# Kernel tuning notes

Measured on AMD Instinct MI355X. Metric: run time of the kernel, lower is better.

## Reference

```python
import jax, jax.numpy as jnp
import numpy as np

EMBED = 512
EXPAND = 1024


def setup_inputs() -> dict:
    key = jax.random.key(0)
    k1, k2, k3, k4, k5 = jax.random.split(key, 5)
    B, C, P, N = 4, EMBED, 16, 1024
    x = jax.random.normal(k1, (B, C, P, N), dtype=jnp.float32)
    # 1x1 conv weights == per-pixel linear maps over the channel dim
    Wqkv = jax.random.normal(k2, (1 + 2 * EXPAND, C), dtype=jnp.float32) * (1.0 / np.sqrt(C))
    bqkv = jax.random.normal(k3, (1 + 2 * EXPAND,), dtype=jnp.float32) * 0.01
    Wout = jax.random.normal(k4, (C, EXPAND), dtype=jnp.float32) * (1.0 / np.sqrt(EXPAND))
    bout = jax.random.normal(k5, (C,), dtype=jnp.float32) * 0.01
    return {"x": x, "Wqkv": Wqkv, "bqkv": bqkv, "Wout": Wout, "bout": bout}


def reference(x, Wqkv, bqkv, Wout, bout):
    # qkv 1x1 conv: (B,C,P,N) -> (B, 1+2E, P, N)
    qkv = jnp.einsum('oc,bcpn->bopn', Wqkv, x) + bqkv[None, :, None, None]
    E = EXPAND
    query = qkv[:, :1]            # (B,1,P,N)
    key_t = qkv[:, 1:1 + E]       # (B,E,P,N)
    value = qkv[:, 1 + E:]        # (B,E,P,N)
    # softmax over patches dim (last axis); attn_dropout p=0.0 -> identity
    context_scores = jax.nn.softmax(query, axis=-1)
    # weighted sum over N, keepdim -> (B,E,P,1)
    context_vector = jnp.sum(key_t * context_scores, axis=-1, keepdims=True)
    # broadcast gate
    out = jax.nn.relu(value) * context_vector  # (B,E,P,N)
    # out 1x1 conv back to embed channels
    out = jnp.einsum('oe,bepn->bopn', Wout, out) + bout[None, :, None, None]
    return out
```

## Files before the change

kernel.cpp:

```cpp
#include <hip/hip_runtime.h>

#define EMBED 512
#define EXPAND 1024
#define PNUM 16
#define NLEN 1024
#define CHW (PNUM * NLEN)
#define SLABS 64

typedef unsigned short u16;
typedef unsigned int u32;
typedef __bf16 bf16x8 __attribute__((ext_vector_type(8)));
typedef u16 u16x8 __attribute__((ext_vector_type(8)));
typedef float f32x4 __attribute__((ext_vector_type(4)));

__device__ __forceinline__ u16 f2bf(float f) {
  u32 u = __builtin_bit_cast(u32, f);
  return (u16)((u + 0x7FFFu + ((u >> 16) & 1u)) >> 16);
}
__device__ __forceinline__ float bf2f(u16 h) {
  return __builtin_bit_cast(float, (u32)h << 16);
}
__device__ __forceinline__ void gld16(const u16* g, u16* l) {
  __builtin_amdgcn_global_load_lds((__attribute__((address_space(1))) void*)g,
                                   (__attribute__((address_space(3))) void*)l,
                                   16, 0, 0);
}
__device__ __forceinline__ f32x4 MFMA(bf16x8 a, bf16x8 b, f32x4 c) {
  return __builtin_amdgcn_mfma_f32_16x16x32_bf16(a, b, c, 0, 0, 0);
}

__global__ __launch_bounds__(256) void k_convert_w(
    const float* __restrict__ Wqkv, const float* __restrict__ Wout,
    u16* __restrict__ WvB, u16* __restrict__ WoutB) {
  const int NV = EXPAND * EMBED;
  int idx = (blockIdx.x * 256 + threadIdx.x) * 4;
  if (idx < NV) {
    float4 v = *(const float4*)(Wqkv + (size_t)(1 + EXPAND) * EMBED + idx);
    uint2 u = make_uint2((u32)f2bf(v.x) | ((u32)f2bf(v.y) << 16),
                         (u32)f2bf(v.z) | ((u32)f2bf(v.w) << 16));
    *(uint2*)(WvB + idx) = u;
  } else {
    int j = idx - NV;
    float4 v = *(const float4*)(Wout + j);
    uint2 u = make_uint2((u32)f2bf(v.x) | ((u32)f2bf(v.y) << 16),
                         (u32)f2bf(v.z) | ((u32)f2bf(v.w) << 16));
    *(uint2*)(WoutB + j) = u;
  }
}

__global__ __launch_bounds__(256) void k_convert_x(
    const float* __restrict__ x, const float* __restrict__ Wqkv,
    float* __restrict__ q, u16* __restrict__ xbT) {
  __shared__ float qp[256];
  const int slab = blockIdx.x >> 4, ng = blockIdx.x & 15;
  const int b = slab >> 4, p = slab & 15;
  const int t = threadIdx.x, w = t >> 6, l = t & 63;
  const int n = ng * 64 + l;
  const float* xs = x + (size_t)b * (EMBED * CHW) + (size_t)p * NLEN + n;
  u16* dst = xbT + (size_t)slab * (NLEN * EMBED) + (size_t)n * EMBED;
  float qacc = 0.f;
  for (int c0 = w * 128; c0 < w * 128 + 128; c0 += 16) {
    u32 pk[8];
#pragma unroll
    for (int j = 0; j < 16; ++j) {
      float v = xs[(size_t)(c0 + j) * CHW];
      qacc += Wqkv[c0 + j] * v;
      u16 h = f2bf(v);
      pk[j >> 1] = (j & 1) ? (pk[j >> 1] | ((u32)h << 16)) : (u32)h;
    }
    uint4* d4 = (uint4*)(dst + c0);
    d4[0] = make_uint4(pk[0], pk[1], pk[2], pk[3]);
    d4[1] = make_uint4(pk[4], pk[5], pk[6], pk[7]);
  }
  qp[t] = qacc;
  __syncthreads();
  if (w == 0) q[(size_t)slab * NLEN + n] = qp[l] + qp[64 + l] + qp[128 + l] + qp[192 + l];
}

__global__ __launch_bounds__(256) void k_attn1(
    const float* __restrict__ q, const u16* __restrict__ xbT,
    float* __restrict__ ypart) {
  __shared__ float red[4];
  __shared__ float sm[256];
  __shared__ float yp[4][512];
  const int slab = blockIdx.x >> 2, qr = blockIdx.x & 3;
  const int t = threadIdx.x, w = t >> 6, l = t & 63;
  const float* qrow = q + (size_t)slab * NLEN;

  float4 q4 = ((const float4*)qrow)[t];
  float m = fmaxf(fmaxf(q4.x, q4.y), fmaxf(q4.z, q4.w));
#pragma unroll
  for (int sh = 32; sh; sh >>= 1) m = fmaxf(m, __shfl_xor(m, sh, 64));
  if (l == 0) red[w] = m;
  __syncthreads();
  float gm = fmaxf(fmaxf(red[0], red[1]), fmaxf(red[2], red[3]));
  float s = __expf(q4.x - gm) + __expf(q4.y - gm) + __expf(q4.z - gm) + __expf(q4.w - gm);
#pragma unroll
  for (int sh = 32; sh; sh >>= 1) s += __shfl_xor(s, sh, 64);
  __syncthreads();
  if (l == 0) red[w] = s;
  __syncthreads();
  float gs = red[0] + red[1] + red[2] + red[3];
  sm[t] = __expf(qrow[qr * 256 + t] - gm) / gs;
  __syncthreads();

  float ya[8] = {0.f, 0.f, 0.f, 0.f, 0.f, 0.f, 0.f, 0.f};
  const u16* xs = xbT + (size_t)slab * (NLEN * EMBED) + (size_t)qr * 256 * EMBED;
  for (int ni = 0; ni < 64; ++ni) {
    const int nloc = ni * 4 + w;
    const float sc = sm[nloc];
    u16x8 v = *(const u16x8*)(xs + (size_t)nloc * EMBED + l * 8);
#pragma unroll
    for (int j = 0; j < 8; ++j) ya[j] += sc * bf2f(v[j]);
  }
#pragma unroll
  for (int j = 0; j < 8; ++j) yp[w][l * 8 + j] = ya[j];
  __syncthreads();
  for (int c = t; c < 512; c += 256)
    ypart[((size_t)slab * 4 + qr) * 512 + c] = yp[0][c] + yp[1][c] + yp[2][c] + yp[3][c];
}

__global__ __launch_bounds__(256) void k_attn2(
    const float* __restrict__ ypart, const float* __restrict__ Wqkv,
    const float* __restrict__ bqkv, float* __restrict__ cv) {
  __shared__ float yl[512];
  const int slab = blockIdx.x >> 2, ec = blockIdx.x & 3;
  const int t = threadIdx.x;
  const int e = ec * 256 + t;
  const float* yb = ypart + (size_t)slab * 4 * 512;
  for (int c = t; c < 512; c += 256)
    yl[c] = yb[c] + yb[512 + c] + yb[1024 + c] + yb[1536 + c];
  __syncthreads();
  const float* wk = Wqkv + (size_t)(1 + e) * EMBED;
  float a = 0.f;
#pragma unroll 4
  for (int c0 = 0; c0 < EMBED; c0 += 4) {
    float4 wv = *(const float4*)(wk + c0);
    a += wv.x * yl[c0] + wv.y * yl[c0 + 1] + wv.z * yl[c0 + 2] + wv.w * yl[c0 + 3];
  }
  cv[(size_t)slab * EXPAND + e] = a + bqkv[1 + e];
}

template <int K, int NT>
__device__ __forceinline__ void gemm256(const u16* __restrict__ Abase,
                                        const u16* __restrict__ Bbase,
                                        u16* lds, f32x4 (&acc)[8][4]) {
  const int t = threadIdx.x;
  const int w = t >> 6, l = t & 63;
  const int wr = w >> 2, wc = w & 3;
  const int lr = l & 15, lj = l >> 4;
  const int rowA0 = wr * 128 + lr;
  const int rowB0 = wc * 64 + lr;

  auto stage = [&](u16* dstBase, const u16* gBase, int kt) {
#pragma unroll
    for (int i = 0; i < 4; ++i) {
      const int s = i * 512 + t;
      const int row = s >> 3;
      const int pch = s & 7;
      gld16(gBase + (size_t)row * K + kt + ((pch ^ (row & 7)) << 3),
            dstBase + s * 8);
    }
  };
  auto rdA = [&](const u16* bufA, int mi, int kc) -> bf16x8 {
    const int row = rowA0 + mi * 16;
    const int ch = kc * 4 + lj;
    return *(const bf16x8*)(bufA + row * 64 + ((ch ^ (row & 7)) << 3));
  };
  auto rdB = [&](const u16* bufB, int ni, int kc) -> bf16x8 {
    const int row = rowB0 + ni * 16;
    const int ch = kc * 4 + lj;
    return *(const bf16x8*)(bufB + row * 64 + ((ch ^ (row & 7)) << 3));
  };

  stage(lds, Abase, 0);
  stage(lds + 16384, Bbase, 0);
  stage(lds + 32768, Abase, 64);
  stage(lds + 49152, Bbase, 64);
  asm volatile("s_waitcnt vmcnt(8)" ::: "memory");
  __builtin_amdgcn_s_barrier();
  __builtin_amdgcn_sched_barrier(0);

#pragma unroll 1
  for (int kt = 0; kt < NT; ++kt) {
    u16* bufA = lds + (kt & 1) * 32768;
    u16* bufB = bufA + 16384;
    const bool st = (kt + 2) < NT;
    const int kt2 = (kt + 2) * 64;
    bf16x8 a0[4][2], a1[4][2], b0[2][2], b1[2][2];

#pragma unroll
    for (int mi = 0; mi < 4; ++mi)
#pragma unroll
      for (int kc = 0; kc < 2; ++kc) a0[mi][kc] = rdA(bufA, mi, kc);
#pragma unroll
    for (int ni = 0; ni < 2; ++ni)
#pragma unroll
      for (int kc = 0; kc < 2; ++kc) b0[ni][kc] = rdB(bufB, ni, kc);
    __builtin_amdgcn_s_barrier();
    __builtin_amdgcn_sched_barrier(0);
    __builtin_amdgcn_s_setprio(1);
#pragma unroll
    for (int mi = 0; mi < 4; ++mi)
#pragma unroll
      for (int ni = 0; ni < 2; ++ni)
#pragma unroll
        for (int kc = 0; kc < 2; ++kc)
          acc[mi][ni] = MFMA(a0[mi][kc], b0[ni][kc], acc[mi][ni]);
    __builtin_amdgcn_s_setprio(0);
    __builtin_amdgcn_sched_barrier(0);
    __builtin_amdgcn_s_barrier();
    __builtin_amdgcn_sched_barrier(0);

#pragma unroll
    for (int ni = 0; ni < 2; ++ni)
#pragma unroll
      for (int kc = 0; kc < 2; ++kc) b1[ni][kc] = rdB(bufB, ni + 2, kc);
    __builtin_amdgcn_s_barrier();
    __builtin_amdgcn_sched_barrier(0);
    __builtin_amdgcn_s_setprio(1);
#pragma unroll
    for (int mi = 0; mi < 4; ++mi)
#pragma unroll
      for (int ni = 0; ni < 2; ++ni)
#pragma unroll
        for (int kc = 0; kc < 2; ++kc)
          acc[mi][ni + 2] = MFMA(a0[mi][kc], b1[ni][kc], acc[mi][ni + 2]);
    __builtin_amdgcn_s_setprio(0);
    __builtin_amdgcn_sched_barrier(0);
    __builtin_amdgcn_s_barrier();
    __builtin_amdgcn_sched_barrier(0);

#pragma unroll
    for (int mi = 0; mi < 4; ++mi)
#pragma unroll
      for (int kc = 0; kc < 2; ++kc) a1[mi][kc] = rdA(bufA, mi + 4, kc);
    if (st) stage(bufB, Bbase, kt2);
    __builtin_amdgcn_s_barrier();
    __builtin_amdgcn_sched_barrier(0);
    __builtin_amdgcn_s_setprio(1);
#pragma unroll
    for (int mi = 0; mi < 4; ++mi)
#pragma unroll
      for (int ni = 0; ni < 2; ++ni)
#pragma unroll
        for (int kc = 0; kc < 2; ++kc)
          acc[mi + 4][ni + 2] = MFMA(a1[mi][kc], b1[ni][kc], acc[mi + 4][ni + 2]);
    __builtin_amdgcn_s_setprio(0);
    __builtin_amdgcn_sched_barrier(0);
    __builtin_amdgcn_s_barrier();
    __builtin_amdgcn_sched_barrier(0);

    if (st) stage(bufA, Abase, kt2);
    __builtin_amdgcn_s_barrier();
    __builtin_amdgcn_sched_barrier(0);
    __builtin_amdgcn_s_setprio(1);
#pragma unroll
    for (int mi = 0; mi < 4; ++mi)
#pragma unroll
      for (int ni = 0; ni < 2; ++ni)
#pragma unroll
        for (int kc = 0; kc < 2; ++kc)
          acc[mi + 4][ni] = MFMA(a1[mi][kc], b0[ni][kc], acc[mi + 4][ni]);
    __builtin_amdgcn_s_setprio(0);
    __builtin_amdgcn_sched_barrier(0);
    if (st)
      asm volatile("s_waitcnt vmcnt(8)" ::: "memory");
    else
      asm volatile("s_waitcnt vmcnt(0)" ::: "memory");
    __builtin_amdgcn_s_barrier();
    __builtin_amdgcn_sched_barrier(0);
  }
}

__global__ __launch_bounds__(512, 2) void k_gemm1(
    const u16* __restrict__ xbT, const u16* __restrict__ WvB,
    const float* __restrict__ bqkv, const float* __restrict__ cv,
    u16* __restrict__ midT) {
  __shared__ __align__(16) u16 lds[65536];
  const int bid = blockIdx.x;
  const int xc = bid & 7, k = bid >> 3;
  const int te = k & 3;
  const int gg = ((k >> 2) << 3) | xc;
  const int slab = gg >> 2, tn = gg & 3;
  const u16* A = xbT + (size_t)slab * (NLEN * EMBED) + (size_t)tn * 256 * EMBED;
  const u16* B = WvB + (size_t)te * 256 * EMBED;
  f32x4 acc[8][4];
  const f32x4 z = {0.f, 0.f, 0.f, 0.f};
#pragma unroll
  for (int i = 0; i < 8; ++i)
#pragma unroll
    for (int j = 0; j < 4; ++j) acc[i][j] = z;
  gemm256<EMBED, 8>(A, B, lds, acc);

  const int t = threadIdx.x, w = t >> 6, l = t & 63;
  const int wr = w >> 2, wc = w & 3;
  const int lr = l & 15, lq4 = (l >> 4) * 4;
#pragma unroll
  for (int ni = 0; ni < 4; ++ni) {
    const int col = wc * 64 + ni * 16 + lr;
    const int e = te * 256 + col;
    const float bv = bqkv[1 + EXPAND + e];
    const float cve = cv[(size_t)slab * EXPAND + e];
#pragma unroll
    for (int mi = 0; mi < 8; ++mi) {
      const int nr = wr * 128 + mi * 16 + lq4;
#pragma unroll
      for (int r = 0; r < 4; ++r) {
        float v = acc[mi][ni][r] + bv;
        v = v > 0.f ? v * cve : 0.f;
        const int row = nr + r;
        lds[row * 256 + ((((col >> 3) ^ (row & 7)) << 3) | (col & 7))] = f2bf(v);
      }
    }
  }
  __syncthreads();
  u16* mt = midT + (size_t)slab * (NLEN * EXPAND) + (size_t)te * 256;
#pragma unroll
  for (int it = 0; it < 16; ++it) {
    const int row = w * 32 + it * 2 + (l >> 5);
    const int ch = (l & 31) ^ (row & 7);
    uint4 v = *(const uint4*)(lds + row * 256 + ch * 8);
    *(uint4*)(mt + (size_t)(tn * 256 + row) * EXPAND + (l & 31) * 8) = v;
  }
}

__global__ __launch_bounds__(512, 2) void k_gemm2(
    const u16* __restrict__ midT, const u16* __restrict__ WoutB,
    const float* __restrict__ bout, float* __restrict__ out) {
  __shared__ __align__(16) u16 lds[65536];
  const int bid = blockIdx.x;
  const int xc = bid & 7, k = bid >> 3;
  const int to = k & 1;
  const int gg = ((k >> 1) << 3) | xc;
  const int slab = gg >> 2, tn = gg & 3;
  const int b = slab >> 4, p = slab & 15;
  const u16* A = midT + (size_t)slab * (NLEN * EXPAND) + (size_t)tn * 256 * EXPAND;
  const u16* B = WoutB + (size_t)to * 256 * EXPAND;
  f32x4 acc[8][4];
  const f32x4 z = {0.f, 0.f, 0.f, 0.f};
#pragma unroll
  for (int i = 0; i < 8; ++i)
#pragma unroll
    for (int j = 0; j < 4; ++j) acc[i][j] = z;
  gemm256<EXPAND, 16>(A, B, lds, acc);

  const int t = threadIdx.x, w = t >> 6, l = t & 63;
  const int wr = w >> 2, wc = w & 3;
  const int lr = l & 15, lq4 = (l >> 4) * 4;
  float* ob = out + (size_t)b * (EMBED * CHW) + (size_t)p * NLEN;
#pragma unroll
  for (int ni = 0; ni < 4; ++ni) {
    const int o = to * 256 + wc * 64 + ni * 16 + lr;
    const float bo = bout[o];
#pragma unroll
    for (int mi = 0; mi < 8; ++mi) {
      const int nr = tn * 256 + wr * 128 + mi * 16 + lq4;
      float4 v;
      v.x = acc[mi][ni][0] + bo;
      v.y = acc[mi][ni][1] + bo;
      v.z = acc[mi][ni][2] + bo;
      v.w = acc[mi][ni][3] + bo;
      *(float4*)(ob + (size_t)o * CHW + nr) = v;
    }
  }
}

extern "C" void kernel_launch(void* const* d_in, const int* in_sizes, int n_in,
                              void* d_out, int out_size, void* d_ws, size_t ws_size,
                              hipStream_t stream) {
  const float* x = (const float*)d_in[0];
  const float* Wqkv = (const float*)d_in[1];
  const float* bqkv = (const float*)d_in[2];
  const float* Wout = (const float*)d_in[3];
  const float* bout = (const float*)d_in[4];
  float* out = (float*)d_out;

  char* ws = (char*)d_ws;
  u16* xbT = (u16*)ws;
  u16* WvB = (u16*)(ws + 67108864);
  u16* WoutB = (u16*)(ws + 68157440);
  float* q = (float*)(ws + 69206016);
  float* cv = (float*)(ws + 69468160);
  u16* midT = (u16*)(ws + 69730304);
  float* ypart = (float*)(ws + 69730304);

  k_convert_w<<<1024, 256, 0, stream>>>(Wqkv, Wout, WvB, WoutB);
  k_convert_x<<<1024, 256, 0, stream>>>(x, Wqkv, q, xbT);
  k_attn1<<<256, 256, 0, stream>>>(q, xbT, ypart);
  k_attn2<<<256, 256, 0, stream>>>(ypart, Wqkv, bqkv, cv);
  k_gemm1<<<1024, 512, 0, stream>>>(xbT, WvB, bqkv, cv, midT);
  k_gemm2<<<512, 512, 0, stream>>>(midT, WoutB, bout, out);
}
```

Before: 300.6 us.

## Transpose x through swizzled LDS tile for coalesced bf16 writes in convert kernel

```diff
diff --git a/kernel.cpp b/kernel.cpp
--- a/kernel.cpp
+++ b/kernel.cpp
@@ -51,30 +51,66 @@
 __global__ __launch_bounds__(256) void k_convert_x(
     const float* __restrict__ x, const float* __restrict__ Wqkv,
     float* __restrict__ q, u16* __restrict__ xbT) {
-  __shared__ float qp[256];
-  const int slab = blockIdx.x >> 4, ng = blockIdx.x & 15;
+  __shared__ __align__(16) u16 tile[128 * 64];
+  __shared__ float qp[256 * 4];
+  const int slab = blockIdx.x >> 3, nw = blockIdx.x & 7;
   const int b = slab >> 4, p = slab & 15;
-  const int t = threadIdx.x, w = t >> 6, l = t & 63;
-  const int n = ng * 64 + l;
-  const float* xs = x + (size_t)b * (EMBED * CHW) + (size_t)p * NLEN + n;
-  u16* dst = xbT + (size_t)slab * (NLEN * EMBED) + (size_t)n * EMBED;
-  float qacc = 0.f;
-  for (int c0 = w * 128; c0 < w * 128 + 128; c0 += 16) {
-    u32 pk[8];
-#pragma unroll
-    for (int j = 0; j < 16; ++j) {
-      float v = xs[(size_t)(c0 + j) * CHW];
-      qacc += Wqkv[c0 + j] * v;
-      u16 h = f2bf(v);
-      pk[j >> 1] = (j & 1) ? (pk[j >> 1] | ((u32)h << 16)) : (u32)h;
-    }
-    uint4* d4 = (uint4*)(dst + c0);
-    d4[0] = make_uint4(pk[0], pk[1], pk[2], pk[3]);
-    d4[1] = make_uint4(pk[4], pk[5], pk[6], pk[7]);
-  }
-  qp[t] = qacc;
-  __syncthreads();
-  if (w == 0) q[(size_t)slab * NLEN + n] = qp[l] + qp[64 + l] + qp[128 + l] + qp[192 + l];
+  const int t = threadIdx.x;
+  const int c8 = t & 7;
+  const int ng = t >> 3;
+  const float* xs = x + (size_t)b * (EMBED * CHW) + (size_t)p * NLEN + nw * 128;
+  u16* dst = xbT + (size_t)slab * (NLEN * EMBED) + (size_t)(nw * 128) * EMBED;
+  float qa[4] = {0.f, 0.f, 0.f, 0.f};
+
+  for (int cc = 0; cc < 8; ++cc) {
+    const int cbase = cc * 64;
+    float4 v[8];
+#pragma unroll
+    for (int k = 0; k < 8; ++k)
+      v[k] = *(const float4*)(xs + (size_t)(cbase + c8 * 8 + k) * CHW + ng * 4);
+    const float* w0 = Wqkv + cbase + c8 * 8;
+#pragma unroll
+    for (int k = 0; k < 8; ++k) {
+      qa[0] += w0[k] * v[k].x;
+      qa[1] += w0[k] * v[k].y;
+      qa[2] += w0[k] * v[k].z;
+      qa[3] += w0[k] * v[k].w;
+    }
+#pragma unroll
+    for (int j = 0; j < 4; ++j) {
+      const int nl = ng * 4 + j;
+      float e[8];
+#pragma unroll
+      for (int k = 0; k < 8; ++k)
+        e[k] = (j == 0) ? v[k].x : (j == 1) ? v[k].y : (j == 2) ? v[k].z : v[k].w;
+      uint4 pk;
+      pk.x = (u32)f2bf(e[0]) | ((u32)f2bf(e[1]) << 16);
+      pk.y = (u32)f2bf(e[2]) | ((u32)f2bf(e[3]) << 16);
+      pk.z = (u32)f2bf(e[4]) | ((u32)f2bf(e[5]) << 16);
+      pk.w = (u32)f2bf(e[6]) | ((u32)f2bf(e[7]) << 16);
+      *(uint4*)(tile + nl * 64 + ((c8 ^ (nl & 7)) << 3)) = pk;
+    }
+    __syncthreads();
+#pragma unroll
+    for (int m = 0; m < 4; ++m) {
+      const int s = m * 256 + t;
+      const int nl = s >> 3, ch = s & 7;
+      uint4 vv = *(const uint4*)(tile + nl * 64 + ((ch ^ (nl & 7)) << 3));
+      *(uint4*)(dst + (size_t)nl * EMBED + cbase + ch * 8) = vv;
+    }
+    __syncthreads();
+  }
+  qp[t * 4 + 0] = qa[0];
+  qp[t * 4 + 1] = qa[1];
+  qp[t * 4 + 2] = qa[2];
+  qp[t * 4 + 3] = qa[3];
+  __syncthreads();
+  if (t < 128) {
+    float a = 0.f;
+#pragma unroll
+    for (int o = 0; o < 8; ++o) a += qp[((((t >> 2) << 3) + o) << 2) + (t & 3)];
+    q[(size_t)slab * NLEN + nw * 128 + t] = a;
+  }
 }
 
 __global__ __launch_bounds__(256) void k_attn1(
@@ -386,7 +422,7 @@
   float* ypart = (float*)(ws + 69730304);
 
   k_convert_w<<<1024, 256, 0, stream>>>(Wqkv, Wout, WvB, WoutB);
-  k_convert_x<<<1024, 256, 0, stream>>>(x, Wqkv, q, xbT);
+  k_convert_x<<<512, 256, 0, stream>>>(x, Wqkv, q, xbT);
   k_attn1<<<256, 256, 0, stream>>>(q, xbT, ypart);
   k_attn2<<<256, 256, 0, stream>>>(ypart, Wqkv, bqkv, cv);
   k_gemm1<<<1024, 512, 0, stream>>>(xbT, WvB, bqkv, cv, midT);
```

New measurement: 267.7 us. 1.12x faster.
